# Kernel optimization log

Hardware: AMD Instinct MI355X
Metric: run time of the kernel (lower is better)

Reference implementation:

```python
import jax, jax.numpy as jnp
import numpy as np

SEMANTIC_DIM = 128
N_COMPONENTS = 2
EMBED_DIM = SEMANTIC_DIM * N_COMPONENTS  # 256
MAX_LEN = 512


def sinusoidal_pe(max_len, d_model):
    pos = jnp.arange(max_len, dtype=jnp.float32)[:, None]              # (L,1)
    div = jnp.exp(jnp.arange(0, d_model, 2, dtype=jnp.float32) * (-np.log(10000.0) / d_model))
    ang = pos * div                                                     # (L, d/2)
    # interleave sin/cos: pe[:,0::2]=sin, pe[:,1::2]=cos
    return jnp.stack([jnp.sin(ang), jnp.cos(ang)], axis=-1).reshape(max_len, d_model)


def setup_inputs() -> dict:
    key = jax.random.key(0)
    k1, k2, k3, k4 = jax.random.split(key, 4)
    byte_sequence = jax.random.randint(k1, (64, 512), 0, 256, dtype=jnp.int64)
    continuous_positions = jax.random.uniform(k2, (64, 2048), dtype=jnp.float32)
    emb_table = jax.random.normal(k3, (256, EMBED_DIM), dtype=jnp.float32)
    locality_shapes = jax.random.normal(k4, (256, 3), dtype=jnp.float32)
    return {
        "byte_sequence": byte_sequence,
        "continuous_positions": continuous_positions,
        "emb_table": emb_table,
        "locality_shapes": locality_shapes,
    }


def reference(byte_sequence, continuous_positions, emb_table, locality_shapes):
    B, L = byte_sequence.shape
    pe = sinusoidal_pe(MAX_LEN, EMBED_DIM)[:L]                          # (L, E)
    byte_embeds = emb_table[byte_sequence] + pe[None, :, :]             # (B, L, E)
    byte_amplitudes = byte_embeds.reshape(B, L, N_COMPONENTS, SEMANTIC_DIM)

    byte_positions = jnp.linspace(0.0, 1.0, L, dtype=jnp.float32)      # (L,)
    x_diff = continuous_positions[:, :, None] - byte_positions[None, None, :]  # (B, P, L)

    lp = locality_shapes[byte_sequence]                                 # (B, L, 3)
    widths = jnp.abs(lp[:, :, 1]) * 0.02 + 1e-5                         # (B, L)
    amplitudes = jax.nn.sigmoid(lp[:, :, 2])                            # (B, L)

    local_basis = jnp.exp(-0.5 * (x_diff / widths[:, None, :]) ** 2) * amplitudes[:, None, :]
    semantic_field = jnp.einsum('bpl,blcd->bpcd', local_basis, byte_amplitudes)
    return semantic_field
```

## Files before the change

### kernel.cpp

```cpp
#include <hip/hip_runtime.h>
#include <math.h>

#define LSEQ 512
#define EDIM 256
#define PDIM 2048
#define BM   128
#define BK   32
#define NT   16

typedef _Float16 f16x8  __attribute__((ext_vector_type(8)));
typedef _Float16 f16x2  __attribute__((ext_vector_type(2)));
typedef float    f32x16 __attribute__((ext_vector_type(16)));

#if __has_builtin(__builtin_amdgcn_exp2f)
#define EXP2F(x) __builtin_amdgcn_exp2f(x)
#else
#define EXP2F(x) __expf((x) * 0.6931471805599453f)
#endif

__device__ inline f16x2 pk2(float a, float b) {
#if __has_builtin(__builtin_amdgcn_cvt_pkrtz)
    return __builtin_bit_cast(f16x2, __builtin_amdgcn_cvt_pkrtz(a, b));
#else
    f16x2 r; r[0] = (_Float16)a; r[1] = (_Float16)b; return r;
#endif
}

__device__ inline float hw_sin(float ang) {
#if __has_builtin(__builtin_amdgcn_sinf)
    float rev = ang * 0.15915494309189535f;
    return __builtin_amdgcn_sinf(rev - floorf(rev));
#else
    return sinf(ang);
#endif
}
__device__ inline float hw_cos(float ang) {
#if __has_builtin(__builtin_amdgcn_cosf)
    float rev = ang * 0.15915494309189535f;
    return __builtin_amdgcn_cosf(rev - floorf(rev));
#else
    return cosf(ang);
#endif
}

__device__ __host__ inline int tile_off(int r, int g) {
    return ((r >> 1) << 6) + ((r & 1) << 5) + (((g ^ ((r >> 1) & 3)) & 3) << 3);
}

__device__ inline void g2lds16(const void* g, void* l) {
    __builtin_amdgcn_global_load_lds(
        (const __attribute__((address_space(1))) void*)g,
        (__attribute__((address_space(3))) void*)l, 16, 0, 0);
}

__global__ __launch_bounds__(256) void precompute_all(
    const int*   __restrict__ bs,
    const float* __restrict__ ls,
    const float* __restrict__ emb,
    float2*      __restrict__ params,
    _Float16*    __restrict__ baset) {
    const int b   = blockIdx.x >> 4;
    const int t   = blockIdx.x & 15;
    const int tid = threadIdx.x;

    __shared__ int sByte[BK];
    if (tid < BK) {
        const int l    = t * BK + tid;
        const int byte = bs[b * LSEQ + l];
        sByte[tid] = byte;
        const float l1  = ls[byte * 3 + 1];
        const float l2  = ls[byte * 3 + 2];
        const float wdt = fabsf(l1) * 0.02f + 1e-5f;
        const float amp = 1.0f / (1.0f + __expf(-l2));
        params[b * LSEQ + l] = make_float2(-0.72134752f / (wdt * wdt),
                                           __log2f(amp));
    }
    __syncthreads();

    const float div = __expf((float)(tid >> 1) * (-2.0f * 9.210340372f / 256.0f));
    _Float16* chunk = baset + ((size_t)blockIdx.x << 13);
#pragma unroll
    for (int g = 0; g < 4; ++g) {
        f16x8 v;
#pragma unroll
        for (int j = 0; j < 8; ++j) {
            const int lj  = g * 8 + j;
            const float ang = (float)(t * BK + lj) * div;
            const float pev = (tid & 1) ? hw_cos(ang) : hw_sin(ang);
            v[j] = (_Float16)(emb[sByte[lj] * EDIM + tid] + pev);
        }
        *(f16x8*)&chunk[tile_off(tid, g)] = v;
    }
}

__global__ __launch_bounds__(512, 4) void field_mfma(
    const float*    __restrict__ cpos,
    const float2*   __restrict__ params,
    const _Float16* __restrict__ baset,
    float*          __restrict__ out) {

    __shared__ __align__(16) _Float16 sW[2][BM * BK];
    __shared__ __align__(16) _Float16 sB[2][EDIM * BK];

    const int orig = blockIdx.x;
    const int wg   = (orig & 7) * 128 + (orig >> 3);
    const int b    = wg >> 4;
    const int pt   = wg & 15;

    const int tid = threadIdx.x, lane = tid & 63, wave = tid >> 6;
    const int l31 = lane & 31, h = lane >> 5;
    const int wrow = wave >> 2, wcol = wave & 3;

    const int sp = tid >> 2;
    const int sg = tid & 3;
    const float mypos = cpos[b * PDIM + pt * BM + sp];
    const float invL  = 1.0f / (float)(LSEQ - 1);
    const int   woff  = tile_off(sp, sg);

    int aoff[2], boff[2];
#pragma unroll
    for (int kk = 0; kk < 2; ++kk) {
        aoff[kk] = tile_off(wrow * 64 + l31, kk * 2 + h);
        boff[kk] = tile_off(wcol * 64 + l31, kk * 2 + h);
    }

    const float2* prm = params + b * LSEQ;
    const _Float16* bt = baset + ((size_t)b * NT << 13);

#pragma unroll
    for (int buf = 0; buf < 2; ++buf) {
        const _Float16* src = bt + buf * 8192 + wave * 1024 + lane * 8;
        g2lds16(src,       &sB[buf][wave * 1024]);
        g2lds16(src + 512, &sB[buf][wave * 1024 + 512]);
    }

    float4 q0, q1, q2, q3;
    {
        const float4* qp = (const float4*)(prm + sg * 8);
        q0 = qp[0]; q1 = qp[1]; q2 = qp[2]; q3 = qp[3];
    }

    auto genW = [&](int t, int dbuf) {
        const float bl0 = (float)(t * BK + sg * 8) * invL;
        const float pd  = mypos - bl0;
        float w[8];
#define GW(i, c2, la) { float d = pd - (float)(i) * invL; \
                        w[i] = EXP2F(fmaf(d * d, (c2), (la))); }
        GW(0, q0.x, q0.y) GW(1, q0.z, q0.w)
        GW(2, q1.x, q1.y) GW(3, q1.z, q1.w)
        GW(4, q2.x, q2.y) GW(5, q2.z, q2.w)
        GW(6, q3.x, q3.y) GW(7, q3.z, q3.w)
#undef GW
        f16x8 wv;
        ((f16x2*)&wv)[0] = pk2(w[0], w[1]);
        ((f16x2*)&wv)[1] = pk2(w[2], w[3]);
        ((f16x2*)&wv)[2] = pk2(w[4], w[5]);
        ((f16x2*)&wv)[3] = pk2(w[6], w[7]);
        *(f16x8*)&sW[dbuf][woff] = wv;
    };

    genW(0, 0);
    __syncthreads();

    f32x16 acc[2][2];
#pragma unroll
    for (int i = 0; i < 2; ++i)
#pragma unroll
        for (int j = 0; j < 2; ++j) acc[i][j] = (f32x16)(0.f);

    for (int t = 0; t < NT; ++t) {
        const int cur = t & 1;

        if (t < NT - 1) {
            const float4* qp = (const float4*)(prm + (t + 1) * BK + sg * 8);
            q0 = qp[0]; q1 = qp[1]; q2 = qp[2]; q3 = qp[3];
        }

        const _Float16* wb_ = sW[cur];
        const _Float16* bb_ = sB[cur];
        __builtin_amdgcn_s_setprio(1);
#pragma unroll
        for (int kk = 0; kk < 2; ++kk) {
            f16x8 fa[2], fb[2];
#pragma unroll
            for (int rt = 0; rt < 2; ++rt) fa[rt] = *(const f16x8*)&wb_[aoff[kk] + rt * 1024];
#pragma unroll
            for (int ct = 0; ct < 2; ++ct) fb[ct] = *(const f16x8*)&bb_[boff[kk] + ct * 1024];
#pragma unroll
            for (int ct = 0; ct < 2; ++ct)
#pragma unroll
                for (int rt = 0; rt < 2; ++rt)
                    acc[rt][ct] = __builtin_amdgcn_mfma_f32_32x32x16_f16(fa[rt], fb[ct], acc[rt][ct], 0, 0, 0);
        }
        __builtin_amdgcn_s_setprio(0);

        if (t < NT - 1) genW(t + 1, cur ^ 1);

        __syncthreads();

        if (t < NT - 2) {
            const _Float16* src = bt + (t + 2) * 8192 + wave * 1024 + lane * 8;
            g2lds16(src,       &sB[cur][wave * 1024]);
            g2lds16(src + 512, &sB[cur][wave * 1024 + 512]);
        }
    }

#pragma unroll
    for (int rt = 0; rt < 2; ++rt)
#pragma unroll
        for (int ct = 0; ct < 2; ++ct) {
            const int e = wcol * 64 + ct * 32 + l31;
            const int pbase = pt * BM + wrow * 64 + rt * 32 + 4 * h;
#pragma unroll
            for (int reg = 0; reg < 16; ++reg) {
                const int p = pbase + (reg & 3) + 8 * (reg >> 2);
                out[((size_t)b * PDIM + p) * EDIM + e] = acc[rt][ct][reg];
            }
        }
}

extern "C" void kernel_launch(void* const* d_in, const int* in_sizes, int n_in,
                              void* d_out, int out_size, void* d_ws, size_t ws_size,
                              hipStream_t stream) {
    const int*   bs   = (const int*)d_in[0];
    const float* cpos = (const float*)d_in[1];
    const float* emb  = (const float*)d_in[2];
    const float* ls   = (const float*)d_in[3];

    const int B = in_sizes[0] / LSEQ;

    char* ws = (char*)d_ws;
    float2*   params = (float2*)ws;
    _Float16* baset  = (_Float16*)(ws + (1u << 18));

    precompute_all<<<B * NT, 256, 0, stream>>>(bs, ls, emb, params, baset);
    field_mfma<<<B * (PDIM / BM), 512, 0, stream>>>(cpos, params, baset, (float*)d_out);
}
```

Before: 76.30 us.

## Generate Gaussian weights directly in MFMA registers and split embedding across blocks

The weight tile is no longer staged through LDS. Each wave computes its f16 weights straight into registers as the A operand of 16x16x32 MFMAs. The embedding dimension is split across two 256-thread workgroups, so each block stages only half of the basis tile, which cuts LDS traffic and barrier coupling. The cost is that the exp-based weight generation is repeated across column waves and across both E-halves, and output stores become narrower 64-byte segments per row.

```diff
diff --git a/kernel.cpp b/kernel.cpp
--- a/kernel.cpp
+++ b/kernel.cpp
@@ -8,9 +8,9 @@
 #define BK   32
 #define NT   16
 
-typedef _Float16 f16x8  __attribute__((ext_vector_type(8)));
-typedef _Float16 f16x2  __attribute__((ext_vector_type(2)));
-typedef float    f32x16 __attribute__((ext_vector_type(16)));
+typedef _Float16 f16x8 __attribute__((ext_vector_type(8)));
+typedef _Float16 f16x2 __attribute__((ext_vector_type(2)));
+typedef float    f32x4 __attribute__((ext_vector_type(4)));
 
 #if __has_builtin(__builtin_amdgcn_exp2f)
 #define EXP2F(x) __builtin_amdgcn_exp2f(x)
@@ -93,39 +93,39 @@
     }
 }
 
-__global__ __launch_bounds__(512, 4) void field_mfma(
+__global__ __launch_bounds__(256, 3) void field_mfma(
     const float*    __restrict__ cpos,
     const float2*   __restrict__ params,
     const _Float16* __restrict__ baset,
     float*          __restrict__ out) {
 
-    __shared__ __align__(16) _Float16 sW[2][BM * BK];
-    __shared__ __align__(16) _Float16 sB[2][EDIM * BK];
+    __shared__ __align__(16) _Float16 sB[2][128 * BK];
 
     const int orig = blockIdx.x;
-    const int wg   = (orig & 7) * 128 + (orig >> 3);
-    const int b    = wg >> 4;
-    const int pt   = wg & 15;
+    const int wg   = (orig & 7) * 256 + (orig >> 3);
+    const int b    = wg >> 5;
+    const int pt   = (wg >> 1) & 15;
+    const int et   = wg & 1;
 
     const int tid = threadIdx.x, lane = tid & 63, wave = tid >> 6;
-    const int l31 = lane & 31, h = lane >> 5;
-    const int wrow = wave >> 2, wcol = wave & 3;
-
-    const int sp = tid >> 2;
-    const int sg = tid & 3;
-    const float mypos = cpos[b * PDIM + pt * BM + sp];
-    const float invL  = 1.0f / (float)(LSEQ - 1);
-    const int   woff  = tile_off(sp, sg);
-
-    int aoff[2], boff[2];
-#pragma unroll
-    for (int kk = 0; kk < 2; ++kk) {
-        aoff[kk] = tile_off(wrow * 64 + l31, kk * 2 + h);
-        boff[kk] = tile_off(wcol * 64 + l31, kk * 2 + h);
-    }
+    const int c15 = lane & 15, g4 = lane >> 4;
+    const int wrow = wave >> 1, wcol = wave & 1;
+
+    const float invL = 1.0f / (float)(LSEQ - 1);
+
+    float pb[4];
+#pragma unroll
+    for (int rt = 0; rt < 4; ++rt)
+        pb[rt] = cpos[b * PDIM + pt * BM + wrow * 64 + rt * 16 + c15]
+                 - (float)(g4 * 8) * invL;
+
+    int boff[4];
+#pragma unroll
+    for (int ct = 0; ct < 4; ++ct)
+        boff[ct] = tile_off(wcol * 64 + ct * 16 + c15, g4);
 
     const float2* prm = params + b * LSEQ;
-    const _Float16* bt = baset + ((size_t)b * NT << 13);
+    const _Float16* bt = baset + (((size_t)b * NT) << 13) + et * 4096;
 
 #pragma unroll
     for (int buf = 0; buf < 2; ++buf) {
@@ -136,65 +136,56 @@
 
     float4 q0, q1, q2, q3;
     {
-        const float4* qp = (const float4*)(prm + sg * 8);
+        const float4* qp = (const float4*)(prm + g4 * 8);
         q0 = qp[0]; q1 = qp[1]; q2 = qp[2]; q3 = qp[3];
     }
-
-    auto genW = [&](int t, int dbuf) {
-        const float bl0 = (float)(t * BK + sg * 8) * invL;
-        const float pd  = mypos - bl0;
-        float w[8];
+    __syncthreads();
+
+    f32x4 acc[4][4];
+#pragma unroll
+    for (int i = 0; i < 4; ++i)
+#pragma unroll
+        for (int j = 0; j < 4; ++j) acc[i][j] = (f32x4)(0.f);
+
+    const float tstep = 32.0f * invL;
+
+    for (int t = 0; t < NT; ++t) {
+        const int cur = t & 1;
+
+        f16x8 af[4];
+        const float tb = (float)t * tstep;
+#pragma unroll
+        for (int rt = 0; rt < 4; ++rt) {
+            const float pd = pb[rt] - tb;
+            float w[8];
 #define GW(i, c2, la) { float d = pd - (float)(i) * invL; \
                         w[i] = EXP2F(fmaf(d * d, (c2), (la))); }
-        GW(0, q0.x, q0.y) GW(1, q0.z, q0.w)
-        GW(2, q1.x, q1.y) GW(3, q1.z, q1.w)
-        GW(4, q2.x, q2.y) GW(5, q2.z, q2.w)
-        GW(6, q3.x, q3.y) GW(7, q3.z, q3.w)
+            GW(0, q0.x, q0.y) GW(1, q0.z, q0.w)
+            GW(2, q1.x, q1.y) GW(3, q1.z, q1.w)
+            GW(4, q2.x, q2.y) GW(5, q2.z, q2.w)
+            GW(6, q3.x, q3.y) GW(7, q3.z, q3.w)
 #undef GW
-        f16x8 wv;
-        ((f16x2*)&wv)[0] = pk2(w[0], w[1]);
-        ((f16x2*)&wv)[1] = pk2(w[2], w[3]);
-        ((f16x2*)&wv)[2] = pk2(w[4], w[5]);
-        ((f16x2*)&wv)[3] = pk2(w[6], w[7]);
-        *(f16x8*)&sW[dbuf][woff] = wv;
-    };
-
-    genW(0, 0);
-    __syncthreads();
-
-    f32x16 acc[2][2];
-#pragma unroll
-    for (int i = 0; i < 2; ++i)
-#pragma unroll
-        for (int j = 0; j < 2; ++j) acc[i][j] = (f32x16)(0.f);
-
-    for (int t = 0; t < NT; ++t) {
-        const int cur = t & 1;
+            ((f16x2*)&af[rt])[0] = pk2(w[0], w[1]);
+            ((f16x2*)&af[rt])[1] = pk2(w[2], w[3]);
+            ((f16x2*)&af[rt])[2] = pk2(w[4], w[5]);
+            ((f16x2*)&af[rt])[3] = pk2(w[6], w[7]);
+        }
 
         if (t < NT - 1) {
-            const float4* qp = (const float4*)(prm + (t + 1) * BK + sg * 8);
+            const float4* qp = (const float4*)(prm + (t + 1) * BK + g4 * 8);
             q0 = qp[0]; q1 = qp[1]; q2 = qp[2]; q3 = qp[3];
         }
 
-        const _Float16* wb_ = sW[cur];
-        const _Float16* bb_ = sB[cur];
+        const _Float16* bb = sB[cur];
         __builtin_amdgcn_s_setprio(1);
 #pragma unroll
-        for (int kk = 0; kk < 2; ++kk) {
-            f16x8 fa[2], fb[2];
-#pragma unroll
-            for (int rt = 0; rt < 2; ++rt) fa[rt] = *(const f16x8*)&wb_[aoff[kk] + rt * 1024];
-#pragma unroll
-            for (int ct = 0; ct < 2; ++ct) fb[ct] = *(const f16x8*)&bb_[boff[kk] + ct * 1024];
-#pragma unroll
-            for (int ct = 0; ct < 2; ++ct)
-#pragma unroll
-                for (int rt = 0; rt < 2; ++rt)
-                    acc[rt][ct] = __builtin_amdgcn_mfma_f32_32x32x16_f16(fa[rt], fb[ct], acc[rt][ct], 0, 0, 0);
+        for (int ct = 0; ct < 4; ++ct) {
+            const f16x8 bf = *(const f16x8*)&bb[boff[ct]];
+#pragma unroll
+            for (int rt = 0; rt < 4; ++rt)
+                acc[rt][ct] = __builtin_amdgcn_mfma_f32_16x16x32_f16(af[rt], bf, acc[rt][ct], 0, 0, 0);
         }
         __builtin_amdgcn_s_setprio(0);
-
-        if (t < NT - 1) genW(t + 1, cur ^ 1);
 
         __syncthreads();
 
@@ -206,14 +197,13 @@
     }
 
 #pragma unroll
-    for (int rt = 0; rt < 2; ++rt)
-#pragma unroll
-        for (int ct = 0; ct < 2; ++ct) {
-            const int e = wcol * 64 + ct * 32 + l31;
-            const int pbase = pt * BM + wrow * 64 + rt * 32 + 4 * h;
-#pragma unroll
-            for (int reg = 0; reg < 16; ++reg) {
-                const int p = pbase + (reg & 3) + 8 * (reg >> 2);
+    for (int rt = 0; rt < 4; ++rt)
+#pragma unroll
+        for (int ct = 0; ct < 4; ++ct) {
+            const int e = et * 128 + wcol * 64 + ct * 16 + c15;
+#pragma unroll
+            for (int reg = 0; reg < 4; ++reg) {
+                const int p = pt * BM + wrow * 64 + rt * 16 + g4 * 4 + reg;
                 out[((size_t)b * PDIM + p) * EDIM + e] = acc[rt][ct][reg];
             }
         }
@@ -234,5 +224,6 @@
     _Float16* baset  = (_Float16*)(ws + (1u << 18));
 
     precompute_all<<<B * NT, 256, 0, stream>>>(bs, ls, emb, params, baset);
-    field_mfma<<<B * (PDIM / BM), 512, 0, stream>>>(cpos, params, baset, (float*)d_out);
-}
+    const int nblocks = B * (PDIM / BM) * 2;
+    field_mfma<<<nblocks, 256, 0, stream>>>(cpos, params, baset, (float*)d_out);
+}
```

Measured after the change: 79.95 us. 1.05x slower.
